# Optimization experiments

Hardware: AMD Instinct MI355X
Metric: run time of the kernel (lower is better)

The kernel has to match this reference:

```python
import jax, jax.numpy as jnp
import numpy as np

D_MODEL = 512
NHEAD = 8
HEAD_DIM = D_MODEL // NHEAD
DFF = 2048
RANK = 64
L = 1024
N = 8
EPS = 1e-5


def _layer_norm(x, g, b):
    m = jnp.mean(x, axis=-1, keepdims=True)
    v = jnp.mean(jnp.square(x - m), axis=-1, keepdims=True)
    return (x - m) * jax.lax.rsqrt(v + EPS) * g + b


def setup_inputs() -> dict:
    key = jax.random.key(0)
    ks = jax.random.split(key, 20)
    s = 1.0 / np.sqrt(D_MODEL)
    inp = {
        "q": jax.random.normal(ks[0], (L, N, D_MODEL), jnp.float32),
        "k": jax.random.normal(ks[1], (L, N, D_MODEL), jnp.float32),
        "v": jax.random.normal(ks[2], (L, N, D_MODEL), jnp.float32),
        # attention projections, stored (in, out) so x @ W
        "Wq": jax.random.normal(ks[3], (D_MODEL, D_MODEL), jnp.float32) * s,
        "bq": jnp.zeros((D_MODEL,), jnp.float32),
        "Wk": jax.random.normal(ks[4], (D_MODEL, D_MODEL), jnp.float32) * s,
        "bk": jnp.zeros((D_MODEL,), jnp.float32),
        "Wv": jax.random.normal(ks[5], (D_MODEL, D_MODEL), jnp.float32) * s,
        "bv": jnp.zeros((D_MODEL,), jnp.float32),
        "Wo": jax.random.normal(ks[6], (D_MODEL, D_MODEL), jnp.float32) * s,
        "bo": jnp.zeros((D_MODEL,), jnp.float32),
        "topk": jnp.float32(0.3),  # learned scalar, k = int(S * sigmoid(topk))
        "A1": jax.random.normal(ks[7], (D_MODEL, RANK), jnp.float32) * s,
        "B1": jax.random.normal(ks[8], (RANK, DFF), jnp.float32) / np.sqrt(RANK),
        "A2": jax.random.normal(ks[9], (DFF, RANK), jnp.float32) / np.sqrt(DFF),
        "B2": jax.random.normal(ks[10], (RANK, D_MODEL), jnp.float32) / np.sqrt(RANK),
        "g1": jnp.ones((D_MODEL,), jnp.float32),
        "be1": jnp.zeros((D_MODEL,), jnp.float32),
        "g2": jnp.ones((D_MODEL,), jnp.float32),
        "be2": jnp.zeros((D_MODEL,), jnp.float32),
    }
    return inp


def reference(q, k, v, Wq, bq, Wk, bk, Wv, bv, Wo, bo, topk,
              A1, B1, A2, B2, g1, be1, g2, be2):
    Lq, Nb, E = q.shape
    S = k.shape[0]
    H, Dh = NHEAD, HEAD_DIM

    # projections -> (N, L, H, Dh)
    qh = (q @ Wq + bq).reshape(Lq, Nb, H, Dh).transpose(1, 0, 2, 3)
    kh = (k @ Wk + bk).reshape(S, Nb, H, Dh).transpose(1, 0, 2, 3)
    vh = (v @ Wv + bv).reshape(S, Nb, H, Dh).transpose(1, 0, 2, 3)

    scores = jnp.einsum('nlhd,nshd->nlhs', qh, kh) / jnp.sqrt(jnp.float32(Dh))

    # dynamic top-k mask: keep the k = int(S * sigmoid(topk)) largest per row
    k_keep = (S * jax.nn.sigmoid(topk)).astype(jnp.int32)  # 588 for topk=0.3
    sorted_desc = jnp.sort(scores, axis=-1)[..., ::-1]
    idx = jnp.broadcast_to(k_keep - 1, scores.shape[:-1])[..., None]
    thresh = jnp.take_along_axis(sorted_desc, idx, axis=-1)  # k-th largest
    masked = jnp.where(scores >= thresh, scores, -jnp.inf)
    attn_w = jax.nn.softmax(masked, axis=-1)

    # note original flattens (d, h) order: 'nlhs,nshd->nldh' then view(L,N,E)
    ao = jnp.einsum('nlhs,nshd->nldh', attn_w, vh)
    ao = ao.transpose(1, 0, 2, 3).reshape(Lq, Nb, E)
    attn_out = ao @ Wo + bo

    src = _layer_norm(q + attn_out, g1, be1)
    ffn = jax.nn.relu(src @ A1 @ B1) @ A2 @ B2
    src = _layer_norm(src + ffn, g2, be2)
    return src
```

## Files before the change

kernel.cpp:

```cpp
#include <hip/hip_runtime.h>

typedef unsigned short u16;
typedef unsigned int u32;
using s16x8 = __attribute__((ext_vector_type(8))) short;
using s16x4 = __attribute__((ext_vector_type(4))) short;
using u16x4 = __attribute__((ext_vector_type(4))) unsigned short;
using u32x4 = __attribute__((ext_vector_type(4))) unsigned int;
using f32x4 = __attribute__((ext_vector_type(4))) float;

__device__ __forceinline__ u16 f2bf(float f) {
  unsigned int u = __float_as_uint(f);
  u += 0x7FFFu + ((u >> 16) & 1u);
  return (u16)(u >> 16);
}
__device__ __forceinline__ float bf2f(u16 b) {
  return __uint_as_float(((u32)b) << 16);
}
__device__ __forceinline__ u32 f2key(float f) {
  u32 u = __float_as_uint(f);
  u32 flip = (u32)((int)u >> 31) | 0x80000000u;
  return (u ^ flip) >> 16;
}
__device__ __forceinline__ float key2f(u32 k) {
  u32 fl = 0x8000u | ((((k >> 15) & 1u) - 1u) & 0x7FFFu);
  return __uint_as_float(((k ^ fl) & 0xFFFFu) << 16);
}

__global__ __launch_bounds__(256) void prep_all(
    const float* __restrict__ q, const float* __restrict__ k, const float* __restrict__ v,
    const float* __restrict__ Wq, const float* __restrict__ Wk, const float* __restrict__ Wv,
    const float* __restrict__ Wo, const float* __restrict__ A1, const float* __restrict__ B1,
    const float* __restrict__ A2, const float* __restrict__ B2,
    u16* __restrict__ qb, u16* __restrict__ kb, u16* __restrict__ vb,
    u16* __restrict__ WqT, u16* __restrict__ WkT, u16* __restrict__ WvT, u16* __restrict__ WoT,
    u16* __restrict__ A1T, u16* __restrict__ B1T, u16* __restrict__ A2T, u16* __restrict__ B2T) {
  int b = blockIdx.x, t = threadIdx.x;
  if (b < 12288) {
    const float* src = b < 4096 ? q : (b < 8192 ? k : v);
    u16* dst = b < 4096 ? qb : (b < 8192 ? kb : vb);
    int i = (b & 4095) * 256 + t;
    float4 f = ((const float4*)src)[i];
    u16x4 o;
    o[0] = f2bf(f.x); o[1] = f2bf(f.y); o[2] = f2bf(f.z); o[3] = f2bf(f.w);
    ((u16x4*)dst)[i] = o;
  } else {
    b -= 12288;
    const float* src; u16* dst; int base, R, C;
    if (b < 1024)      { src = Wq; dst = WqT; base = 0;    R = 512;  C = 512; }
    else if (b < 2048) { src = Wk; dst = WkT; base = 1024; R = 512;  C = 512; }
    else if (b < 3072) { src = Wv; dst = WvT; base = 2048; R = 512;  C = 512; }
    else if (b < 4096) { src = Wo; dst = WoT; base = 3072; R = 512;  C = 512; }
    else if (b < 4224) { src = A1; dst = A1T; base = 4096; R = 512;  C = 64;  }
    else if (b < 4736) { src = B1; dst = B1T; base = 4224; R = 64;   C = 2048;}
    else if (b < 5248) { src = A2; dst = A2T; base = 4736; R = 2048; C = 64;  }
    else               { src = B2; dst = B2T; base = 5248; R = 64;   C = 512; }
    int idx = (b - base) * 256 + t;
    int r = idx / C, c = idx % C;
    dst[(size_t)c * R + r] = f2bf(src[idx]);
  }
}

__global__ __launch_bounds__(256, 4) void qkv_fused(
    const u16* __restrict__ qb, const u16* __restrict__ kb, const u16* __restrict__ vb,
    const u16* __restrict__ WqT, const u16* __restrict__ WkT, const u16* __restrict__ WvT,
    const float* __restrict__ bq, const float* __restrict__ bk, const float* __restrict__ bv,
    u16* __restrict__ Qw, u16* __restrict__ Kw, u16* __restrict__ Vw) {
  __shared__ __align__(16) u16 As[128][72];
  __shared__ __align__(16) u16 Bs[128][72];
  const int z = blockIdx.z;
  const u16* A = z == 0 ? qb : (z == 1 ? kb : vb);
  const u16* Bt = z == 0 ? WqT : (z == 1 ? WkT : WvT);
  const float* bias = z == 0 ? bq : (z == 1 ? bk : bv);
  u16* outp = z == 0 ? Qw : (z == 1 ? Kw : Vw);

  const int tid = threadIdx.x;
  const int m0 = blockIdx.y * 128, n0 = blockIdx.x * 128;
  const int lane = tid & 63, wid = tid >> 6;
  const int l16 = lane & 15, hi = lane >> 4;
  const int wr = (wid >> 1) * 64, wc = (wid & 1) * 64;

  f32x4 acc[4][4];
#pragma unroll
  for (int i = 0; i < 4; ++i)
#pragma unroll
    for (int j = 0; j < 4; ++j) acc[i][j] = (f32x4){0.f, 0.f, 0.f, 0.f};

  for (int k0 = 0; k0 < 512; k0 += 64) {
    if (k0) __syncthreads();
#pragma unroll
    for (int i = 0; i < 4; ++i) {
      int idx = i * 256 + tid;
      int r = idx >> 3, cc = (idx & 7) * 8;
      *(s16x8*)&As[r][cc] = *(const s16x8*)&A[(size_t)(m0 + r) * 512 + k0 + cc];
      *(s16x8*)&Bs[r][cc] = *(const s16x8*)&Bt[(size_t)(n0 + r) * 512 + k0 + cc];
    }
    __syncthreads();
#pragma unroll
    for (int kk = 0; kk < 2; ++kk) {
      const int kb_ = kk * 32 + hi * 8;
      s16x8 af[4], bf[4];
#pragma unroll
      for (int mf = 0; mf < 4; ++mf) af[mf] = *(const s16x8*)&As[wr + mf * 16 + l16][kb_];
#pragma unroll
      for (int nf = 0; nf < 4; ++nf) bf[nf] = *(const s16x8*)&Bs[wc + nf * 16 + l16][kb_];
#pragma unroll
      for (int mf = 0; mf < 4; ++mf)
#pragma unroll
        for (int nf = 0; nf < 4; ++nf)
          acc[mf][nf] = __builtin_amdgcn_mfma_f32_16x16x32_bf16(af[mf], bf[nf], acc[mf][nf], 0, 0, 0);
    }
  }

#pragma unroll
  for (int mf = 0; mf < 4; ++mf)
#pragma unroll
    for (int nf = 0; nf < 4; ++nf)
#pragma unroll
      for (int i = 0; i < 4; ++i) {
        int row = m0 + wr + mf * 16 + hi * 4 + i;
        int col = n0 + wc + nf * 16 + l16;
        float val = acc[mf][nf][i] + bias[col];
        if (z == 0) val *= 0.125f;
        int l = row >> 3, n = row & 7, hh = col >> 6, d = col & 63;
        if (z < 2)
          outp[(((size_t)(n * 8 + hh) * 1024 + l) << 6) + d] = f2bf(val);
        else
          outp[((size_t)(n * 8 + hh) * 64 + d) * 1024 + l] = f2bf(val);
      }
}

__global__ __launch_bounds__(512, 4) void attn_kernel(const u16* __restrict__ Qw,
                                                      const u16* __restrict__ Kw,
                                                      const u16* __restrict__ Vw,
                                                      const float* __restrict__ topk,
                                                      u16* __restrict__ ao) {
  __shared__ __align__(16) u16 scb[32 * 1024];
  __shared__ __align__(16) u16 Qt[32][72];
  __shared__ float invs[32];
  const int tid = threadIdx.x, lane = tid & 63, wid = tid >> 6;
  const int l16 = lane & 15, hi = lane >> 4;
  const int mb = blockIdx.x, nh = blockIdx.y;

  const int kkeep = (int)(1024.f / (1.f + __expf(-topk[0])));

  {
    int r = tid >> 4, dc = (tid & 15) << 2;
    *(s16x4*)&Qt[r][dc] =
        *(const s16x4*)&Qw[((size_t)nh * 1024 + mb * 32 + r) * 64 + dc];
  }
  __syncthreads();

  {
    const u16* Kb = Kw + (size_t)nh * 1024 * 64;
    s16x8 bq0[2], bq1[2];
#pragma unroll
    for (int qh = 0; qh < 2; ++qh) {
      bq0[qh] = *(const s16x8*)&Qt[qh * 16 + l16][hi * 8];
      bq1[qh] = *(const s16x8*)&Qt[qh * 16 + l16][32 + hi * 8];
    }
    const int s0 = wid * 128;
#pragma unroll
    for (int nf = 0; nf < 8; ++nf) {
      const int sr = s0 + nf * 16 + l16;
      s16x8 a0 = *(const s16x8*)&Kb[(size_t)sr * 64 + hi * 8];
      s16x8 a1 = *(const s16x8*)&Kb[(size_t)sr * 64 + 32 + hi * 8];
#pragma unroll
      for (int qh = 0; qh < 2; ++qh) {
        f32x4 acc = {0.f, 0.f, 0.f, 0.f};
        acc = __builtin_amdgcn_mfma_f32_16x16x32_bf16(a0, bq0[qh], acc, 0, 0, 0);
        acc = __builtin_amdgcn_mfma_f32_16x16x32_bf16(a1, bq1[qh], acc, 0, 0, 0);
        const int row_q = qh * 16 + l16;
        u32 k0 = f2key(acc[0]) | (f2key(acc[1]) << 16);
        u32 k1 = f2key(acc[2]) | (f2key(acc[3]) << 16);
        char* rowq = (char*)scb + row_q * 2048;
        int boff = (2 * (s0 + nf * 16 + 4 * hi)) ^ ((row_q & 7) << 4);
        *(uint2*)(rowq + boff) = make_uint2(k0, k1);
      }
    }
  }
  __syncthreads();

  {
    const int row = wid * 4 + hi;
    const int Xr = (row & 7) << 4;
    char* rowb = (char*)scb + row * 2048;
    u32 dp[32];
#pragma unroll
    for (int c = 0; c < 8; ++c) {
      u32x4 w4 = *(const u32x4*)(rowb + ((16 * l16 + 256 * c) ^ Xr));
#pragma unroll
      for (int t = 0; t < 4; ++t) dp[4 * c + t] = (w4[t] & 0xFFFEFFFEu) >> 1;
    }

    u32 T = 0;
#pragma unroll
    for (int bit = 14; bit >= 0; --bit) {
      u32 cand = T + (1u << bit);
      u32 cc = 0x80008000u - ((cand << 16) | cand);
      u32 acc = 0;
#pragma unroll
      for (int i = 0; i < 32; ++i) acc += ((dp[i] + cc) >> 15) & 0x00010001u;
      int cnt = (int)((acc & 0xFFFFu) + (acc >> 16));
      cnt += __shfl_xor(cnt, 1); cnt += __shfl_xor(cnt, 2);
      cnt += __shfl_xor(cnt, 4); cnt += __shfl_xor(cnt, 8);
      if (cnt >= kkeep) T = cand;
    }

    u32 mx = 0;
#pragma unroll
    for (int i = 0; i < 32; ++i) mx = max(mx, max(dp[i] << 16, dp[i] & 0xFFFF0000u));
    mx = max(mx, (u32)__shfl_xor((int)mx, 1));
    mx = max(mx, (u32)__shfl_xor((int)mx, 2));
    mx = max(mx, (u32)__shfl_xor((int)mx, 4));
    mx = max(mx, (u32)__shfl_xor((int)mx, 8));
    const float mval = key2f((mx >> 16) << 1);
    const u32 T2 = T << 1;

    float sum = 0.f;
#pragma unroll
    for (int c = 0; c < 8; ++c) {
      char* p = rowb + ((16 * l16 + 256 * c) ^ Xr);
      u32x4 w4 = *(const u32x4*)p;
      u32 outw[4];
#pragma unroll
      for (int t = 0; t < 4; ++t) {
        u32 w = w4[t];
        u32 tlo = w << 16;
        u32 thi = w & 0xFFFF0000u;
        u32 flo = ((int)tlo < 0) ? 0x80000000u : 0xFFFF0000u;
        u32 fhi = ((int)thi < 0) ? 0x80000000u : 0xFFFF0000u;
        float vlo = __uint_as_float(tlo ^ flo);
        float vhi = __uint_as_float(thi ^ fhi);
        float elo = ((w & 0xFFFFu) >= T2) ? __expf(vlo - mval) : 0.f;
        float ehi = ((w >> 16) >= T2) ? __expf(vhi - mval) : 0.f;
        sum += elo + ehi;
        u32 pk;
        asm("v_cvt_pk_bf16_f32 %0, %1, %2" : "=v"(pk) : "v"(elo), "v"(ehi));
        outw[t] = pk;
      }
      *(u32x4*)p = *(u32x4*)outw;
    }
    sum += __shfl_xor(sum, 1); sum += __shfl_xor(sum, 2);
    sum += __shfl_xor(sum, 4); sum += __shfl_xor(sum, 8);
    if (l16 == 0) invs[row] = __builtin_amdgcn_rcpf(sum);
  }
  __syncthreads();

  {
    const u16* Vb = Vw + (size_t)nh * 64 * 1024;
    const int rh = wid >> 2, d0 = (wid & 3) * 16;
    f32x4 oacc0 = {0.f, 0.f, 0.f, 0.f};
    f32x4 oacc1 = {0.f, 0.f, 0.f, 0.f};
    const char* Pbase = (const char*)scb + (rh * 16 + l16) * 2048;
    const int Xp = (l16 & 7) << 4;
#pragma unroll
    for (int ks = 0; ks < 32; ks += 2) {
      int kb0 = (ks * 64 + hi * 16) ^ Xp;
      int kb1 = ((ks + 1) * 64 + hi * 16) ^ Xp;
      s16x8 a0 = *(const s16x8*)(Pbase + kb0);
      s16x8 a1 = *(const s16x8*)(Pbase + kb1);
      s16x8 b0 = *(const s16x8*)&Vb[(size_t)(d0 + l16) * 1024 + ks * 32 + hi * 8];
      s16x8 b1 = *(const s16x8*)&Vb[(size_t)(d0 + l16) * 1024 + (ks + 1) * 32 + hi * 8];
      oacc0 = __builtin_amdgcn_mfma_f32_16x16x32_bf16(a0, b0, oacc0, 0, 0, 0);
      oacc1 = __builtin_amdgcn_mfma_f32_16x16x32_bf16(a1, b1, oacc1, 0, 0, 0);
    }
    const int n = nh >> 3, hh = nh & 7;
#pragma unroll
    for (int i = 0; i < 4; ++i) {
      int l = mb * 32 + rh * 16 + hi * 4 + i;
      int d = d0 + l16;
      float vv = (oacc0[i] + oacc1[i]) * invs[rh * 16 + hi * 4 + i];
      ao[(size_t)(l * 8 + n) * 512 + d * 8 + hh] = f2bf(vv);
    }
  }
}

template <bool FIRST>
__global__ __launch_bounds__(256, 2) void gemm_ln(const u16* __restrict__ A,
                                                  const u16* __restrict__ Bt,
                                                  const float* __restrict__ bias,
                                                  const float* __restrict__ residf,
                                                  const u16* __restrict__ residb,
                                                  const float* __restrict__ g,
                                                  const float* __restrict__ be,
                                                  float* __restrict__ outf,
                                                  u16* __restrict__ outb) {
  constexpr int K = FIRST ? 512 : 64;
  __shared__ __align__(16) u16 As[16][72];
  __shared__ float red_s[4][16];
  __shared__ float red_q[4][16];
  const int tid = threadIdx.x;
  const int lane = tid & 63, wid = tid >> 6;
  const int l16 = lane & 15, hi = lane >> 4;
  const int m0 = blockIdx.x * 16;
  const int wc = wid * 128;

  f32x4 acc[8];
#pragma unroll
  for (int nf = 0; nf < 8; ++nf) acc[nf] = (f32x4){0.f, 0.f, 0.f, 0.f};

  for (int k0 = 0; k0 < K; k0 += 64) {
    if (k0) __syncthreads();
    {
      int r = tid >> 4, c = (tid & 15) << 2;
      *(s16x4*)&As[r][c] = *(const s16x4*)&A[(size_t)(m0 + r) * K + k0 + c];
    }
    __syncthreads();
#pragma unroll
    for (int kk = 0; kk < 2; ++kk) {
      const int kb_ = kk * 32 + hi * 8;
      s16x8 a = *(const s16x8*)&As[l16][kb_];
#pragma unroll
      for (int nf = 0; nf < 8; ++nf) {
        s16x8 b = *(const s16x8*)&Bt[(size_t)(wc + nf * 16 + l16) * K + k0 + kb_];
        acc[nf] = __builtin_amdgcn_mfma_f32_16x16x32_bf16(a, b, acc[nf], 0, 0, 0);
      }
    }
  }

#pragma unroll
  for (int nf = 0; nf < 8; ++nf) {
    int col = wc + nf * 16 + l16;
#pragma unroll
    for (int i = 0; i < 4; ++i) {
      float v = acc[nf][i];
      int row = m0 + hi * 4 + i;
      if (FIRST) v += bias[col] + residf[(size_t)row * 512 + col];
      else v += bf2f(residb[(size_t)row * 512 + col]);
      acc[nf][i] = v;
    }
  }
  float s[4] = {0.f, 0.f, 0.f, 0.f}, q2[4] = {0.f, 0.f, 0.f, 0.f};
#pragma unroll
  for (int nf = 0; nf < 8; ++nf)
#pragma unroll
    for (int i = 0; i < 4; ++i) {
      s[i] += acc[nf][i];
      q2[i] += acc[nf][i] * acc[nf][i];
    }
#pragma unroll
  for (int i = 0; i < 4; ++i) {
#pragma unroll
    for (int off = 1; off < 16; off <<= 1) {
      s[i] += __shfl_xor(s[i], off);
      q2[i] += __shfl_xor(q2[i], off);
    }
  }
  if (l16 == 0) {
#pragma unroll
    for (int i = 0; i < 4; ++i) {
      red_s[wid][hi * 4 + i] = s[i];
      red_q[wid][hi * 4 + i] = q2[i];
    }
  }
  __syncthreads();
  float mean[4], rstd[4];
#pragma unroll
  for (int i = 0; i < 4; ++i) {
    int r = hi * 4 + i;
    float ms = red_s[0][r] + red_s[1][r] + red_s[2][r] + red_s[3][r];
    float mq = red_q[0][r] + red_q[1][r] + red_q[2][r] + red_q[3][r];
    mean[i] = ms * (1.f / 512.f);
    float var = mq * (1.f / 512.f) - mean[i] * mean[i];
    rstd[i] = rsqrtf(var + 1e-5f);
  }
#pragma unroll
  for (int nf = 0; nf < 8; ++nf) {
    int col = wc + nf * 16 + l16;
    float gv = g[col], bev = be[col];
#pragma unroll
    for (int i = 0; i < 4; ++i) {
      int row = m0 + hi * 4 + i;
      float y = (acc[nf][i] - mean[i]) * rstd[i] * gv + bev;
      if (FIRST) outb[(size_t)row * 512 + col] = f2bf(y);
      else outf[(size_t)row * 512 + col] = y;
    }
  }
}

__global__ __launch_bounds__(256, 4) void ffn3(const u16* __restrict__ srcb,
                                               const u16* __restrict__ A1T,
                                               const u16* __restrict__ B1T,
                                               const u16* __restrict__ A2T,
                                               u16* __restrict__ w2) {
  __shared__ __align__(16) u16 As[32][72];
  __shared__ __align__(16) u16 Bs[64][72];
  __shared__ __align__(16) u16 Us[32][72];
  __shared__ __align__(16) u16 B1s[64][72];
  __shared__ __align__(16) u16 A2s[64][72];
  __shared__ __align__(16) u16 Hs[32][72];
  const int tid = threadIdx.x;
  const int lane = tid & 63, wid = tid >> 6;
  const int l16 = lane & 15, hi = lane >> 4;
  const int m0 = blockIdx.x * 32;
  const int wm = (wid & 1) * 16, wn = (wid >> 1) * 32;

  f32x4 accu[2];
  accu[0] = (f32x4){0.f, 0.f, 0.f, 0.f};
  accu[1] = (f32x4){0.f, 0.f, 0.f, 0.f};
  for (int k0 = 0; k0 < 512; k0 += 64) {
    if (k0) __syncthreads();
    {
      int r = tid >> 3, c = (tid & 7) << 3;
      *(s16x8*)&As[r][c] = *(const s16x8*)&srcb[(size_t)(m0 + r) * 512 + k0 + c];
    }
#pragma unroll
    for (int i = 0; i < 2; ++i) {
      int idx = i * 256 + tid;
      int r = idx >> 3, c = (idx & 7) << 3;
      *(s16x8*)&Bs[r][c] = *(const s16x8*)&A1T[(size_t)r * 512 + k0 + c];
    }
    __syncthreads();
#pragma unroll
    for (int kk = 0; kk < 2; ++kk) {
      const int kb_ = kk * 32 + hi * 8;
      s16x8 a = *(const s16x8*)&As[wm + l16][kb_];
#pragma unroll
      for (int j = 0; j < 2; ++j) {
        s16x8 b = *(const s16x8*)&Bs[wn + j * 16 + l16][kb_];
        accu[j] = __builtin_amdgcn_mfma_f32_16x16x32_bf16(a, b, accu[j], 0, 0, 0);
      }
    }
  }
  __syncthreads();
#pragma unroll
  for (int j = 0; j < 2; ++j)
#pragma unroll
    for (int i = 0; i < 4; ++i)
      Us[wm + hi * 4 + i][wn + j * 16 + l16] = f2bf(accu[j][i]);

  f32x4 w2a[2];
  w2a[0] = (f32x4){0.f, 0.f, 0.f, 0.f};
  w2a[1] = (f32x4){0.f, 0.f, 0.f, 0.f};
  for (int jc = 0; jc < 32; ++jc) {
#pragma unroll
    for (int i = 0; i < 2; ++i) {
      int idx = i * 256 + tid;
      int r = idx >> 3, c = (idx & 7) << 3;
      *(s16x8*)&B1s[r][c] = *(const s16x8*)&B1T[(size_t)(jc * 64 + r) * 64 + c];
      *(s16x8*)&A2s[r][c] = *(const s16x8*)&A2T[(size_t)r * 2048 + jc * 64 + c];
    }
    __syncthreads();
    f32x4 ha[2];
    ha[0] = (f32x4){0.f, 0.f, 0.f, 0.f};
    ha[1] = (f32x4){0.f, 0.f, 0.f, 0.f};
#pragma unroll
    for (int kk = 0; kk < 2; ++kk) {
      const int kb_ = kk * 32 + hi * 8;
      s16x8 a = *(const s16x8*)&Us[wm + l16][kb_];
#pragma unroll
      for (int j = 0; j < 2; ++j) {
        s16x8 b = *(const s16x8*)&B1s[wn + j * 16 + l16][kb_];
        ha[j] = __builtin_amdgcn_mfma_f32_16x16x32_bf16(a, b, ha[j], 0, 0, 0);
      }
    }
#pragma unroll
    for (int j = 0; j < 2; ++j)
#pragma unroll
      for (int i = 0; i < 4; ++i)
        Hs[wm + hi * 4 + i][wn + j * 16 + l16] = f2bf(fmaxf(ha[j][i], 0.f));
    __syncthreads();
#pragma unroll
    for (int kk = 0; kk < 2; ++kk) {
      const int kb_ = kk * 32 + hi * 8;
      s16x8 a = *(const s16x8*)&Hs[wm + l16][kb_];
#pragma unroll
      for (int j = 0; j < 2; ++j) {
        s16x8 b = *(const s16x8*)&A2s[wn + j * 16 + l16][kb_];
        w2a[j] = __builtin_amdgcn_mfma_f32_16x16x32_bf16(a, b, w2a[j], 0, 0, 0);
      }
    }
    __syncthreads();
  }
#pragma unroll
  for (int j = 0; j < 2; ++j)
#pragma unroll
    for (int i = 0; i < 4; ++i)
      w2[(size_t)(m0 + wm + hi * 4 + i) * 64 + wn + j * 16 + l16] = f2bf(w2a[j][i]);
}

extern "C" void kernel_launch(void* const* d_in, const int* in_sizes, int n_in,
                              void* d_out, int out_size, void* d_ws, size_t ws_size,
                              hipStream_t stream) {
  const float* q = (const float*)d_in[0];
  const float* k = (const float*)d_in[1];
  const float* v = (const float*)d_in[2];
  const float* Wq = (const float*)d_in[3];
  const float* bq = (const float*)d_in[4];
  const float* Wk = (const float*)d_in[5];
  const float* bk = (const float*)d_in[6];
  const float* Wv = (const float*)d_in[7];
  const float* bv = (const float*)d_in[8];
  const float* Wo = (const float*)d_in[9];
  const float* bo = (const float*)d_in[10];
  const float* topk = (const float*)d_in[11];
  const float* A1 = (const float*)d_in[12];
  const float* B1 = (const float*)d_in[13];
  const float* A2 = (const float*)d_in[14];
  const float* B2 = (const float*)d_in[15];
  const float* g1 = (const float*)d_in[16];
  const float* be1 = (const float*)d_in[17];
  const float* g2 = (const float*)d_in[18];
  const float* be2 = (const float*)d_in[19];

  char* ws = (char*)d_ws;
  constexpr size_t SZ_TOK_BF = (size_t)8192 * 512 * 2;
  constexpr size_t SZ_W_BF = (size_t)512 * 512 * 2;
  constexpr size_t O_QB = 0;
  constexpr size_t O_KB = O_QB + SZ_TOK_BF;
  constexpr size_t O_VB = O_KB + SZ_TOK_BF;
  constexpr size_t O_QW = O_VB + SZ_TOK_BF;
  constexpr size_t O_KW = O_QW + SZ_TOK_BF;
  constexpr size_t O_VW = O_KW + SZ_TOK_BF;
  constexpr size_t O_WQT = O_VW + SZ_TOK_BF;
  constexpr size_t O_WKT = O_WQT + SZ_W_BF;
  constexpr size_t O_WVT = O_WKT + SZ_W_BF;
  constexpr size_t O_WOT = O_WVT + SZ_W_BF;
  constexpr size_t O_A1T = O_WOT + SZ_W_BF;
  constexpr size_t O_B1T = O_A1T + 65536;
  constexpr size_t O_A2T = O_B1T + 262144;
  constexpr size_t O_B2T = O_A2T + 262144;
  constexpr size_t O_AO = O_B2T + 65536;
  constexpr size_t O_SRCB = O_AO + SZ_TOK_BF;
  constexpr size_t O_W2 = O_SRCB + SZ_TOK_BF;

  u16* qb = (u16*)(ws + O_QB);
  u16* kb = (u16*)(ws + O_KB);
  u16* vb = (u16*)(ws + O_VB);
  u16* Qw_ = (u16*)(ws + O_QW);
  u16* Kw_ = (u16*)(ws + O_KW);
  u16* Vw_ = (u16*)(ws + O_VW);
  u16* WqT = (u16*)(ws + O_WQT);
  u16* WkT = (u16*)(ws + O_WKT);
  u16* WvT = (u16*)(ws + O_WVT);
  u16* WoT = (u16*)(ws + O_WOT);
  u16* A1T = (u16*)(ws + O_A1T);
  u16* B1T = (u16*)(ws + O_B1T);
  u16* A2T = (u16*)(ws + O_A2T);
  u16* B2T = (u16*)(ws + O_B2T);
  u16* ao = (u16*)(ws + O_AO);
  u16* srcb = (u16*)(ws + O_SRCB);
  u16* w2 = (u16*)(ws + O_W2);

  prep_all<<<17664, 256, 0, stream>>>(q, k, v, Wq, Wk, Wv, Wo, A1, B1, A2, B2,
                                      qb, kb, vb, WqT, WkT, WvT, WoT, A1T, B1T, A2T, B2T);

  qkv_fused<<<dim3(4, 64, 3), 256, 0, stream>>>(qb, kb, vb, WqT, WkT, WvT,
                                                bq, bk, bv, Qw_, Kw_, Vw_);

  attn_kernel<<<dim3(32, 64), 512, 0, stream>>>(Qw_, Kw_, Vw_, topk, ao);

  gemm_ln<true><<<512, 256, 0, stream>>>(ao, WoT, bo, q, nullptr, g1, be1, nullptr, srcb);

  ffn3<<<256, 256, 0, stream>>>(srcb, A1T, B1T, A2T, w2);

  gemm_ln<false><<<512, 256, 0, stream>>>(w2, B2T, nullptr, nullptr, srcb, g2, be2,
                                          (float*)d_out, nullptr);
}
```

Baseline: 282.0 us.

## Fuse fp32-to-bf16 activation conversion into QKV GEMM and rewrite top-k selection with ballots

Drops the separate pass that converted q/k/v to bf16 in workspace. The QKV GEMM now reads fp32 activations directly and packs them to bf16 while staging tiles into shared memory, removing one full write and read of three 8 MB tensors. The top-k threshold search in attention is also restructured: each wave handles two full rows, counts with ballot/popcount across 64 lanes instead of packed 16-bit SWAR counting, and uses the threshold rather than the row max as the softmax offset. The GEMM now loads twice as many bytes per tile, and the new binary search runs 16 bits with wider reductions.

```diff
diff --git a/kernel.cpp b/kernel.cpp
--- a/kernel.cpp
+++ b/kernel.cpp
@@ -16,59 +16,52 @@
 __device__ __forceinline__ float bf2f(u16 b) {
   return __uint_as_float(((u32)b) << 16);
 }
+__device__ __forceinline__ u32 pkbf(float a, float b) {
+  u32 r;
+  asm("v_cvt_pk_bf16_f32 %0, %1, %2" : "=v"(r) : "v"(a), "v"(b));
+  return r;
+}
 __device__ __forceinline__ u32 f2key(float f) {
   u32 u = __float_as_uint(f);
   u32 flip = (u32)((int)u >> 31) | 0x80000000u;
   return (u ^ flip) >> 16;
 }
 __device__ __forceinline__ float key2f(u32 k) {
-  u32 fl = 0x8000u | ((((k >> 15) & 1u) - 1u) & 0x7FFFu);
-  return __uint_as_float(((k ^ fl) & 0xFFFFu) << 16);
-}
-
-__global__ __launch_bounds__(256) void prep_all(
-    const float* __restrict__ q, const float* __restrict__ k, const float* __restrict__ v,
+  u32 t = k << 16;
+  u32 msk = ((int)t < 0) ? 0x80000000u : 0xFFFF0000u;
+  return __uint_as_float(t ^ msk);
+}
+
+__global__ __launch_bounds__(256) void prep_w(
     const float* __restrict__ Wq, const float* __restrict__ Wk, const float* __restrict__ Wv,
     const float* __restrict__ Wo, const float* __restrict__ A1, const float* __restrict__ B1,
     const float* __restrict__ A2, const float* __restrict__ B2,
-    u16* __restrict__ qb, u16* __restrict__ kb, u16* __restrict__ vb,
     u16* __restrict__ WqT, u16* __restrict__ WkT, u16* __restrict__ WvT, u16* __restrict__ WoT,
     u16* __restrict__ A1T, u16* __restrict__ B1T, u16* __restrict__ A2T, u16* __restrict__ B2T) {
   int b = blockIdx.x, t = threadIdx.x;
-  if (b < 12288) {
-    const float* src = b < 4096 ? q : (b < 8192 ? k : v);
-    u16* dst = b < 4096 ? qb : (b < 8192 ? kb : vb);
-    int i = (b & 4095) * 256 + t;
-    float4 f = ((const float4*)src)[i];
-    u16x4 o;
-    o[0] = f2bf(f.x); o[1] = f2bf(f.y); o[2] = f2bf(f.z); o[3] = f2bf(f.w);
-    ((u16x4*)dst)[i] = o;
-  } else {
-    b -= 12288;
-    const float* src; u16* dst; int base, R, C;
-    if (b < 1024)      { src = Wq; dst = WqT; base = 0;    R = 512;  C = 512; }
-    else if (b < 2048) { src = Wk; dst = WkT; base = 1024; R = 512;  C = 512; }
-    else if (b < 3072) { src = Wv; dst = WvT; base = 2048; R = 512;  C = 512; }
-    else if (b < 4096) { src = Wo; dst = WoT; base = 3072; R = 512;  C = 512; }
-    else if (b < 4224) { src = A1; dst = A1T; base = 4096; R = 512;  C = 64;  }
-    else if (b < 4736) { src = B1; dst = B1T; base = 4224; R = 64;   C = 2048;}
-    else if (b < 5248) { src = A2; dst = A2T; base = 4736; R = 2048; C = 64;  }
-    else               { src = B2; dst = B2T; base = 5248; R = 64;   C = 512; }
-    int idx = (b - base) * 256 + t;
-    int r = idx / C, c = idx % C;
-    dst[(size_t)c * R + r] = f2bf(src[idx]);
-  }
+  const float* src; u16* dst; int base, R, C;
+  if (b < 1024)      { src = Wq; dst = WqT; base = 0;    R = 512;  C = 512; }
+  else if (b < 2048) { src = Wk; dst = WkT; base = 1024; R = 512;  C = 512; }
+  else if (b < 3072) { src = Wv; dst = WvT; base = 2048; R = 512;  C = 512; }
+  else if (b < 4096) { src = Wo; dst = WoT; base = 3072; R = 512;  C = 512; }
+  else if (b < 4224) { src = A1; dst = A1T; base = 4096; R = 512;  C = 64;  }
+  else if (b < 4736) { src = B1; dst = B1T; base = 4224; R = 64;   C = 2048;}
+  else if (b < 5248) { src = A2; dst = A2T; base = 4736; R = 2048; C = 64;  }
+  else               { src = B2; dst = B2T; base = 5248; R = 64;   C = 512; }
+  int idx = (b - base) * 256 + t;
+  int r = idx / C, c = idx % C;
+  dst[(size_t)c * R + r] = f2bf(src[idx]);
 }
 
 __global__ __launch_bounds__(256, 4) void qkv_fused(
-    const u16* __restrict__ qb, const u16* __restrict__ kb, const u16* __restrict__ vb,
+    const float* __restrict__ q, const float* __restrict__ k, const float* __restrict__ v,
     const u16* __restrict__ WqT, const u16* __restrict__ WkT, const u16* __restrict__ WvT,
     const float* __restrict__ bq, const float* __restrict__ bk, const float* __restrict__ bv,
     u16* __restrict__ Qw, u16* __restrict__ Kw, u16* __restrict__ Vw) {
   __shared__ __align__(16) u16 As[128][72];
   __shared__ __align__(16) u16 Bs[128][72];
   const int z = blockIdx.z;
-  const u16* A = z == 0 ? qb : (z == 1 ? kb : vb);
+  const float* A = z == 0 ? q : (z == 1 ? k : v);
   const u16* Bt = z == 0 ? WqT : (z == 1 ? WkT : WvT);
   const float* bias = z == 0 ? bq : (z == 1 ? bk : bv);
   u16* outp = z == 0 ? Qw : (z == 1 ? Kw : Vw);
@@ -91,7 +84,12 @@
     for (int i = 0; i < 4; ++i) {
       int idx = i * 256 + tid;
       int r = idx >> 3, cc = (idx & 7) * 8;
-      *(s16x8*)&As[r][cc] = *(const s16x8*)&A[(size_t)(m0 + r) * 512 + k0 + cc];
+      float4 f0 = *(const float4*)&A[(size_t)(m0 + r) * 512 + k0 + cc];
+      float4 f1 = *(const float4*)&A[(size_t)(m0 + r) * 512 + k0 + cc + 4];
+      u32x4 pk;
+      pk[0] = pkbf(f0.x, f0.y); pk[1] = pkbf(f0.z, f0.w);
+      pk[2] = pkbf(f1.x, f1.y); pk[3] = pkbf(f1.z, f1.w);
+      *(u32x4*)&As[r][cc] = pk;
       *(s16x8*)&Bs[r][cc] = *(const s16x8*)&Bt[(size_t)(n0 + r) * 512 + k0 + cc];
     }
     __syncthreads();
@@ -181,68 +179,65 @@
   __syncthreads();
 
   {
-    const int row = wid * 4 + hi;
-    const int Xr = (row & 7) << 4;
-    char* rowb = (char*)scb + row * 2048;
-    u32 dp[32];
-#pragma unroll
-    for (int c = 0; c < 8; ++c) {
-      u32x4 w4 = *(const u32x4*)(rowb + ((16 * l16 + 256 * c) ^ Xr));
-#pragma unroll
-      for (int t = 0; t < 4; ++t) dp[4 * c + t] = (w4[t] & 0xFFFEFFFEu) >> 1;
-    }
-
-    u32 T = 0;
-#pragma unroll
-    for (int bit = 14; bit >= 0; --bit) {
-      u32 cand = T + (1u << bit);
-      u32 cc = 0x80008000u - ((cand << 16) | cand);
-      u32 acc = 0;
-#pragma unroll
-      for (int i = 0; i < 32; ++i) acc += ((dp[i] + cc) >> 15) & 0x00010001u;
-      int cnt = (int)((acc & 0xFFFFu) + (acc >> 16));
-      cnt += __shfl_xor(cnt, 1); cnt += __shfl_xor(cnt, 2);
-      cnt += __shfl_xor(cnt, 4); cnt += __shfl_xor(cnt, 8);
-      if (cnt >= kkeep) T = cand;
-    }
-
-    u32 mx = 0;
-#pragma unroll
-    for (int i = 0; i < 32; ++i) mx = max(mx, max(dp[i] << 16, dp[i] & 0xFFFF0000u));
-    mx = max(mx, (u32)__shfl_xor((int)mx, 1));
-    mx = max(mx, (u32)__shfl_xor((int)mx, 2));
-    mx = max(mx, (u32)__shfl_xor((int)mx, 4));
-    mx = max(mx, (u32)__shfl_xor((int)mx, 8));
-    const float mval = key2f((mx >> 16) << 1);
-    const u32 T2 = T << 1;
-
-    float sum = 0.f;
-#pragma unroll
-    for (int c = 0; c < 8; ++c) {
-      char* p = rowb + ((16 * l16 + 256 * c) ^ Xr);
-      u32x4 w4 = *(const u32x4*)p;
-      u32 outw[4];
-#pragma unroll
-      for (int t = 0; t < 4; ++t) {
-        u32 w = w4[t];
-        u32 tlo = w << 16;
-        u32 thi = w & 0xFFFF0000u;
-        u32 flo = ((int)tlo < 0) ? 0x80000000u : 0xFFFF0000u;
-        u32 fhi = ((int)thi < 0) ? 0x80000000u : 0xFFFF0000u;
-        float vlo = __uint_as_float(tlo ^ flo);
-        float vhi = __uint_as_float(thi ^ fhi);
-        float elo = ((w & 0xFFFFu) >= T2) ? __expf(vlo - mval) : 0.f;
-        float ehi = ((w >> 16) >= T2) ? __expf(vhi - mval) : 0.f;
-        sum += elo + ehi;
-        u32 pk;
-        asm("v_cvt_pk_bf16_f32 %0, %1, %2" : "=v"(pk) : "v"(elo), "v"(ehi));
-        outw[t] = pk;
-      }
-      *(u32x4*)p = *(u32x4*)outw;
-    }
-    sum += __shfl_xor(sum, 1); sum += __shfl_xor(sum, 2);
-    sum += __shfl_xor(sum, 4); sum += __shfl_xor(sum, 8);
-    if (l16 == 0) invs[row] = __builtin_amdgcn_rcpf(sum);
+#pragma unroll
+    for (int rp = 0; rp < 2; ++rp) {
+      const int r0 = wid * 4 + rp * 2, r1 = r0 + 1;
+      char* rb0 = (char*)scb + r0 * 2048;
+      char* rb1 = (char*)scb + r1 * 2048;
+      const int X0 = (r0 & 7) << 4, X1 = (r1 & 7) << 4;
+      u32 ka[16], kb_[16];
+#pragma unroll
+      for (int c = 0; c < 8; ++c) {
+        u32 wa = *(const u32*)(rb0 + ((4 * lane + 256 * c) ^ X0));
+        u32 wb = *(const u32*)(rb1 + ((4 * lane + 256 * c) ^ X1));
+        ka[2 * c] = wa & 0xFFFFu; ka[2 * c + 1] = wa >> 16;
+        kb_[2 * c] = wb & 0xFFFFu; kb_[2 * c + 1] = wb >> 16;
+      }
+      u32 Ta = 0, Tb = 0;
+#pragma unroll
+      for (int bit = 15; bit >= 0; --bit) {
+        u32 ca = Ta + (1u << bit), cb = Tb + (1u << bit);
+        int na = 0, nb = 0;
+#pragma unroll
+        for (int j = 0; j < 16; ++j) {
+          na += __popcll(__ballot(ka[j] >= ca));
+          nb += __popcll(__ballot(kb_[j] >= cb));
+        }
+        if (na >= kkeep) Ta = ca;
+        if (nb >= kkeep) Tb = cb;
+      }
+      const float tva = key2f(Ta), tvb = key2f(Tb);
+      float suma = 0.f, sumb = 0.f;
+#pragma unroll
+      for (int c = 0; c < 8; ++c) {
+        float ea0, ea1, eb0, eb1;
+        {
+          u32 kk0 = ka[2 * c], kk1 = ka[2 * c + 1];
+          float v0 = key2f(kk0), v1 = key2f(kk1);
+          ea0 = (kk0 >= Ta) ? __expf(v0 - tva) : 0.f;
+          ea1 = (kk1 >= Ta) ? __expf(v1 - tva) : 0.f;
+          suma += ea0 + ea1;
+        }
+        {
+          u32 kk0 = kb_[2 * c], kk1 = kb_[2 * c + 1];
+          float v0 = key2f(kk0), v1 = key2f(kk1);
+          eb0 = (kk0 >= Tb) ? __expf(v0 - tvb) : 0.f;
+          eb1 = (kk1 >= Tb) ? __expf(v1 - tvb) : 0.f;
+          sumb += eb0 + eb1;
+        }
+        *(u32*)(rb0 + ((4 * lane + 256 * c) ^ X0)) = pkbf(ea0, ea1);
+        *(u32*)(rb1 + ((4 * lane + 256 * c) ^ X1)) = pkbf(eb0, eb1);
+      }
+#pragma unroll
+      for (int off = 1; off < 64; off <<= 1) {
+        suma += __shfl_xor(suma, off);
+        sumb += __shfl_xor(sumb, off);
+      }
+      if (lane == 0) {
+        invs[r0] = __builtin_amdgcn_rcpf(suma);
+        invs[r1] = __builtin_amdgcn_rcpf(sumb);
+      }
+    }
   }
   __syncthreads();
 
@@ -506,10 +501,7 @@
   char* ws = (char*)d_ws;
   constexpr size_t SZ_TOK_BF = (size_t)8192 * 512 * 2;
   constexpr size_t SZ_W_BF = (size_t)512 * 512 * 2;
-  constexpr size_t O_QB = 0;
-  constexpr size_t O_KB = O_QB + SZ_TOK_BF;
-  constexpr size_t O_VB = O_KB + SZ_TOK_BF;
-  constexpr size_t O_QW = O_VB + SZ_TOK_BF;
+  constexpr size_t O_QW = 0;
   constexpr size_t O_KW = O_QW + SZ_TOK_BF;
   constexpr size_t O_VW = O_KW + SZ_TOK_BF;
   constexpr size_t O_WQT = O_VW + SZ_TOK_BF;
@@ -524,9 +516,6 @@
   constexpr size_t O_SRCB = O_AO + SZ_TOK_BF;
   constexpr size_t O_W2 = O_SRCB + SZ_TOK_BF;
 
-  u16* qb = (u16*)(ws + O_QB);
-  u16* kb = (u16*)(ws + O_KB);
-  u16* vb = (u16*)(ws + O_VB);
   u16* Qw_ = (u16*)(ws + O_QW);
   u16* Kw_ = (u16*)(ws + O_KW);
   u16* Vw_ = (u16*)(ws + O_VW);
@@ -542,10 +531,10 @@
   u16* srcb = (u16*)(ws + O_SRCB);
   u16* w2 = (u16*)(ws + O_W2);
 
-  prep_all<<<17664, 256, 0, stream>>>(q, k, v, Wq, Wk, Wv, Wo, A1, B1, A2, B2,
-                                      qb, kb, vb, WqT, WkT, WvT, WoT, A1T, B1T, A2T, B2T);
-
-  qkv_fused<<<dim3(4, 64, 3), 256, 0, stream>>>(qb, kb, vb, WqT, WkT, WvT,
+  prep_w<<<5376, 256, 0, stream>>>(Wq, Wk, Wv, Wo, A1, B1, A2, B2,
+                                   WqT, WkT, WvT, WoT, A1T, B1T, A2T, B2T);
+
+  qkv_fused<<<dim3(4, 64, 3), 256, 0, stream>>>(q, k, v, WqT, WkT, WvT,
                                                 bq, bk, bv, Qw_, Kw_, Vw_);
 
   attn_kernel<<<dim3(32, 64), 512, 0, stream>>>(Qw_, Kw_, Vw_, topk, ao);
```

Result: no change. 286.0 us (+1.4%).
